# Optimization experiments

Measured on AMD Instinct MI355X. Metric: run time of the kernel, lower is better.

Reference implementation:

```python
import jax, jax.numpy as jnp
import numpy as np

N = 65536      # detector nodes (hits)
P = 128        # particles
DIM = 3
N_NEAREST = 5
EPS = 1e-8
BIG = 999.0


def setup_inputs() -> dict:
    key = jax.random.key(0)
    ks = jax.random.split(key, 9)
    x = jax.random.normal(ks[0], (N, DIM), jnp.float32)
    q = jax.random.uniform(ks[1], (N,), jnp.float32)
    is_cond_point = (jax.random.uniform(ks[2], (N,)) < 0.2).astype(jnp.float32)
    beta = jax.random.uniform(ks[3], (N,), jnp.float32)
    node_class = jax.random.randint(ks[4], (N,), 0, 6).astype(jnp.float32)
    max_x = jax.random.normal(ks[5], (P, DIM), jnp.float32)
    max_q = jax.random.uniform(ks[6], (P,), jnp.float32) + 0.5
    particle_class = jax.random.randint(ks[7], (P,), 0, 6).astype(jnp.float32)
    parent_target = jax.random.randint(ks[8], (N,), 0, P, dtype=jnp.int32)
    particle_idx = jnp.arange(P, dtype=jnp.int32)
    return dict(x=x, q=q, is_cond_point=is_cond_point, beta=beta,
                node_class=node_class, max_x=max_x, max_q=max_q,
                particle_class=particle_class, parent_target=parent_target,
                particle_idx=particle_idx)


def _rms_stats(dx, dxq, belongs, q_mailbox, cond_dist):
    # dx/dxq/belongs/cond_dist: [C, N] mailboxes (C receivers, each sees all N nodes)
    Np = belongs.sum(axis=1)                                   # [C]
    rms = jnp.sqrt(jnp.sum((dx * belongs) ** 2, axis=1) / Np)
    sum_q = jnp.sum(q_mailbox)  # NOTE: original sums the ENTIRE mailbox (quirk kept)
    rmsq = jnp.sqrt(jnp.sum(dxq ** 2, axis=1) / (Np * sum_q))
    cond = jnp.where(cond_dist < EPS, BIG, cond_dist)
    nn = -jax.lax.top_k(-cond, N_NEAREST)[0]  # 5 smallest, ascending == sort+slice
    return rms, rmsq, Np, nn


def reference(x, q, is_cond_point, beta, node_class, max_x, max_q, particle_class,
              parent_target, particle_idx):
    # --- update_all node_to_particle (message_dist -> compute_rms) ---
    dx = jnp.linalg.norm(x[None, :, :] - max_x[:, None, :], axis=-1)          # [P,N]
    belongs = (parent_target[None, :] == particle_idx[:, None]).astype(dx.dtype)
    dxq = dx * q[None, :] * max_q[:, None]
    cond = dx * is_cond_point[None, :]
    q_mb = jnp.broadcast_to(q[None, :], dx.shape)
    rms, rmsq, Np, nn = _rms_stats(dx, dxq, belongs, q_mb, cond)

    # --- update_all nodes->global (dst lacks 'max x'/'max q'/'particle idx') ---
    dxg = jnp.linalg.norm(x, axis=-1)[None, :]                                # [1,N]
    dxqg = dxg * q[None, :]
    belongs_g = jnp.ones_like(dxg)
    cond_g = dxg * is_cond_point[None, :]
    rms_g, rmsq_g, Ng, nn_g = _rms_stats(dxg, dxqg, belongs_g, q[None, :], cond_g)

    # --- update_all particles->global: Davies-Bouldin over [P,P] pairs ---
    DS = rms[:, None] + rms[None, :]                                          # Si+Sj
    M2 = jnp.sum((max_x[:, None, :] - max_x[None, :, :]) ** 2, axis=-1)       # ||xi-xj||^2
    R = jnp.where(M2 > 0, DS / jnp.where(M2 > 0, M2, 1.0), 0.0)               # nan/inf->0
    db = jnp.mean(jnp.max(R, axis=1))                                         # (1/P) sum_i max_j

    # --- update_all particle_to_node: node inherits its parent particle's N ---
    N_node = jnp.einsum('pn,p->n', belongs, Np)                               # [N]

    # --- apply_edges particle_to_node: ||max_x_p - x_n|| and membership ---
    dist_edge = dx            # [P,N], identical math to edges' 'dist x'
    belongs_edge = belongs    # [P,N]; beta/class edge feats are pure broadcasts

    return (rms, rmsq, Np, nn, rms_g, rmsq_g, Ng, nn_g, db,
            N_node, dist_edge, belongs_edge)
```

## Files before the change

### kernel.cpp

```cpp
#include <hip/hip_runtime.h>

#define NN 65536
#define PP 128
#define EPSV 1e-8f
#define BIGV 999.0f
#define MAGIC 0x7FEDC123

typedef float f32x4 __attribute__((ext_vector_type(4)));
typedef int   i32x4 __attribute__((ext_vector_type(4)));

#define O_RMS   0
#define O_RMSQ  128
#define O_NP    256
#define O_NN    384
#define O_RMSG  1024
#define O_RMSQG 1025
#define O_NG    1026
#define O_NNG   1027
#define O_DB    1032
#define O_NNODE 1033
#define O_DIST  66569
#define O_BEL   (66569 + 8388608)

#define W_BS   0
#define W_PP   512
#define W_CNT  41472
#define W_FLG  41536
#define W_CL4  41600

__device__ inline float wred(float v) {
#pragma unroll
  for (int o = 32; o > 0; o >>= 1) v += __shfl_down(v, o, 64);
  return v;
}

__device__ inline void t5ins(float t[5], float v) {
  if (v < t[4]) {
    t[4] = v;
#pragma unroll
    for (int k = 4; k > 0; --k)
      if (t[k] < t[k - 1]) { float tm = t[k]; t[k] = t[k - 1]; t[k - 1] = tm; }
  }
}

__device__ inline void merge5(const float* a, const float* b, float* o) {
  int i = 0, j = 0;
#pragma unroll
  for (int k = 0; k < 5; ++k) {
    float av = a[i], bv = b[j];
    if (av <= bv) { o[k] = av; ++i; } else { o[k] = bv; ++j; }
  }
}

__device__ inline void spin_flags(const int* flg, int tid) {
  if (tid < 64) {
    while (__hip_atomic_load(flg + tid, __ATOMIC_ACQUIRE,
                             __HIP_MEMORY_SCOPE_AGENT) != MAGIC)
      __builtin_amdgcn_s_sleep(2);
  }
  __syncthreads();
}

__global__ __launch_bounds__(256, 5) void gA(const float* __restrict__ x,
                                             const float* __restrict__ q,
                                             const float* __restrict__ ic,
                                             const int* __restrict__ par,
                                             const float* __restrict__ mx,
                                             const float* __restrict__ mq,
                                             float* __restrict__ ws,
                                             float* __restrict__ out) {
  __shared__ __align__(16) float sbuf[4132];
  int tid = threadIdx.x, bx = blockIdx.x;
  int* flg = (int*)ws + W_FLG;
  if (bx < 64) {
    float* ps = sbuf;
    float* wsum = sbuf + 640;
    int* swc = (int*)(sbuf + 672);
    int b = bx;
    for (int i = tid; i < 640; i += 256) ps[i] = 0.f;
    __syncthreads();
    float A = 0.f, B0 = 0.f, B1 = 0.f, B2 = 0.f, Cq = 0.f, Sq = 0.f, Sxx = 0.f;
    float4* cl4 = (float4*)(ws + W_CL4);
    int base = b * 1024;
    int wv = tid >> 6, lane = tid & 63;
    int running = 0;
    int pas[4];
#pragma unroll
    for (int it = 0; it < 4; ++it) {
      int n = base + it * 256 + tid;
      float x0 = x[3 * n], x1 = x[3 * n + 1], x2 = x[3 * n + 2];
      float qn = q[n], icn = ic[n];
      int pa = par[n];
      pas[it] = pa;
      float xx = fmaf(x0, x0, fmaf(x1, x1, x2 * x2));
      float q2 = qn * qn;
      A = fmaf(q2, xx, A); B0 = fmaf(q2, x0, B0);
      B1 = fmaf(q2, x1, B1); B2 = fmaf(q2, x2, B2);
      Cq += q2; Sq += qn; Sxx += xx;
      atomicAdd(&ps[pa], x0);
      atomicAdd(&ps[128 + pa], x1);
      atomicAdd(&ps[256 + pa], x2);
      atomicAdd(&ps[384 + pa], xx);
      atomicAdd(&ps[512 + pa], 1.0f);
      bool has = (icn != 0.0f);
      unsigned long long m = __ballot(has);
      if (lane == 0) swc[wv] = __popcll(m);
      __syncthreads();
      int c0 = swc[0], c1 = swc[1], c2 = swc[2], c3 = swc[3];
      int wbase = running + ((wv > 0) ? c0 : 0) + ((wv > 1) ? c1 : 0) + ((wv > 2) ? c2 : 0);
      if (has) {
        int pre = __popcll(m & ((1ull << lane) - 1ull));
        cl4[base + wbase + pre] = make_float4(x0, x1, x2, icn);
      }
      running += c0 + c1 + c2 + c3;
      __syncthreads();
    }
    A = wred(A); B0 = wred(B0); B1 = wred(B1); B2 = wred(B2);
    Cq = wred(Cq); Sq = wred(Sq); Sxx = wred(Sxx);
    if (lane == 0) {
      wsum[wv * 8 + 0] = A; wsum[wv * 8 + 1] = B0; wsum[wv * 8 + 2] = B1;
      wsum[wv * 8 + 3] = B2; wsum[wv * 8 + 4] = Cq; wsum[wv * 8 + 5] = Sq;
      wsum[wv * 8 + 6] = Sxx;
    }
    __syncthreads();
    if (tid < 7)
      ws[W_BS + b * 8 + tid] =
          wsum[tid] + wsum[8 + tid] + wsum[16 + tid] + wsum[24 + tid];
    if (tid == 0) ((int*)ws)[W_CNT + b] = running;
    for (int i = tid; i < 640; i += 256) ws[W_PP + b * 640 + i] = ps[i];
    __threadfence();
    __syncthreads();
    if (tid == 0)
      __hip_atomic_store(flg + b, MAGIC, __ATOMIC_RELEASE, __HIP_MEMORY_SCOPE_AGENT);
    spin_flags(flg, tid);
    float* snp = sbuf;
    if (tid < 128) {
      float s = 0.f;
      for (int b2 = 0; b2 < 64; ++b2) s += ws[W_PP + b2 * 640 + 512 + tid];
      snp[tid] = s;
    }
    __syncthreads();
#pragma unroll
    for (int it = 0; it < 4; ++it) {
      int n = base + it * 256 + tid;
      __builtin_nontemporal_store(snp[pas[it]], out + O_NNODE + n);
    }
  } else if (bx < 1088) {
    float* sx = sbuf;
    int* spar = (int*)(sbuf + 3080);
    float* smx = sbuf + 4108;
    int e = bx - 64;
    int ey = e >> 6, ex = e & 63;
    int p0 = ey * 8;
    if (tid < 24) smx[tid] = mx[p0 * 3 + tid];
    for (int i = tid; i < 770; i += 256) {
      int g4 = 768 * ex + 2 + i;
      if (g4 < 49152) *(f32x4*)(sx + 4 * i) = ((const f32x4*)x)[g4];
    }
    for (int i = tid; i < 257; i += 256) {
      int g4 = 256 * ex + i;
      if (g4 < 16384) *(i32x4*)(spar + 4 * i) = ((const i32x4*)par)[g4];
    }
    __syncthreads();
    int v = ex * 256 + tid;
    if (v < 16383) {
      int n0 = 3 + 4 * v;
      int lx = 1 + 12 * tid;
      float xv[12];
#pragma unroll
      for (int j = 0; j < 12; ++j) xv[j] = sx[lx + j];
      int lp = 3 + 4 * tid;
      int pa0 = spar[lp], pa1 = spar[lp + 1], pa2 = spar[lp + 2], pa3 = spar[lp + 3];
#pragma unroll
      for (int pi = 0; pi < 8; ++pi) {
        int p = p0 + pi;
        float m0 = smx[3 * pi], m1 = smx[3 * pi + 1], m2 = smx[3 * pi + 2];
        f32x4 d, bl;
        float d0, d1, d2;
        d0 = xv[0] - m0; d1 = xv[1] - m1; d2 = xv[2] - m2;
        d.x = sqrtf(fmaf(d0, d0, fmaf(d1, d1, d2 * d2)));
        d0 = xv[3] - m0; d1 = xv[4] - m1; d2 = xv[5] - m2;
        d.y = sqrtf(fmaf(d0, d0, fmaf(d1, d1, d2 * d2)));
        d0 = xv[6] - m0; d1 = xv[7] - m1; d2 = xv[8] - m2;
        d.z = sqrtf(fmaf(d0, d0, fmaf(d1, d1, d2 * d2)));
        d0 = xv[9] - m0; d1 = xv[10] - m1; d2 = xv[11] - m2;
        d.w = sqrtf(fmaf(d0, d0, fmaf(d1, d1, d2 * d2)));
        bl.x = (pa0 == p) ? 1.f : 0.f; bl.y = (pa1 == p) ? 1.f : 0.f;
        bl.z = (pa2 == p) ? 1.f : 0.f; bl.w = (pa3 == p) ? 1.f : 0.f;
        size_t ro = (size_t)p * NN + n0;
        __builtin_nontemporal_store(d,  (f32x4*)(out + O_DIST + ro));
        __builtin_nontemporal_store(bl, (f32x4*)(out + O_BEL + ro));
      }
    } else if (v == 16383) {
      float xs[4][3];
      int pa_r[4];
      int ns[4] = {0, 1, 2, 65535};
#pragma unroll
      for (int k = 0; k < 3; ++k) {
        xs[k][0] = x[3 * k]; xs[k][1] = x[3 * k + 1]; xs[k][2] = x[3 * k + 2];
        pa_r[k] = par[k];
      }
      xs[3][0] = sx[3061]; xs[3][1] = sx[3062]; xs[3][2] = sx[3063];
      pa_r[3] = spar[1023];
#pragma unroll
      for (int k = 0; k < 4; ++k) {
#pragma unroll
        for (int pi = 0; pi < 8; ++pi) {
          int p = p0 + pi;
          float m0 = smx[3 * pi], m1 = smx[3 * pi + 1], m2 = smx[3 * pi + 2];
          float d0 = xs[k][0] - m0, d1 = xs[k][1] - m1, d2 = xs[k][2] - m2;
          float dd = sqrtf(fmaf(d0, d0, fmaf(d1, d1, d2 * d2)));
          size_t ro = (size_t)p * NN + ns[k];
          __builtin_nontemporal_store(dd, out + O_DIST + ro);
          __builtin_nontemporal_store((pa_r[k] == p) ? 1.f : 0.f, out + O_BEL + ro);
        }
      }
    }
  } else {
    int r = bx - 1088;
    spin_flags(flg, tid);
    if (r < 129) {
      int* cnts = (int*)sbuf;
      float* sl = sbuf + 64;
      float m0 = 0.f, m1 = 0.f, m2 = 0.f;
      if (r < 128) { m0 = mx[3 * r]; m1 = mx[3 * r + 1]; m2 = mx[3 * r + 2]; }
      if (tid < 64) cnts[tid] = ((const int*)ws)[W_CNT + tid];
      __syncthreads();
      const float4* cl4 = (const float4*)(ws + W_CL4);
      float t[5] = {BIGV, BIGV, BIGV, BIGV, BIGV};
      for (int seg = 0; seg < 64; ++seg) {
        int c = cnts[seg];
        for (int i = tid; i < c; i += 256) {
          float4 e = cl4[seg * 1024 + i];
          float d0 = e.x - m0, d1 = e.y - m1, d2 = e.z - m2;
          float dd = sqrtf(fmaf(d0, d0, fmaf(d1, d1, d2 * d2)));
          float vv = dd * e.w;
          vv = (vv < EPSV) ? BIGV : vv;
          t5ins(t, vv);
        }
      }
#pragma unroll
      for (int k = 0; k < 5; ++k) sl[tid * 5 + k] = t[k];
      __syncthreads();
      for (int s = 128; s >= 1; s >>= 1) {
        if (tid < s) {
          float a[5], b[5], o[5];
#pragma unroll
          for (int k = 0; k < 5; ++k) { a[k] = sl[tid * 5 + k]; b[k] = sl[(tid + s) * 5 + k]; }
          merge5(a, b, o);
#pragma unroll
          for (int k = 0; k < 5; ++k) sl[tid * 5 + k] = o[k];
        }
        __syncthreads();
      }
      if (tid == 0) {
        float* dst = (r < 128) ? (out + O_NN + 5 * r) : (out + O_NNG);
#pragma unroll
        for (int k = 0; k < 5; ++k) dst[k] = sl[k];
      }
    } else {
      float* gs = sbuf;
      float* srms = sbuf + 8;
      float* smx2 = sbuf + 136;
      float* wsum2 = sbuf + 520;
      if (tid < 64) {
        float a0 = ws[W_BS + tid * 8 + 0], a1 = ws[W_BS + tid * 8 + 1];
        float a2 = ws[W_BS + tid * 8 + 2], a3 = ws[W_BS + tid * 8 + 3];
        float a4 = ws[W_BS + tid * 8 + 4], a5 = ws[W_BS + tid * 8 + 5];
        float a6 = ws[W_BS + tid * 8 + 6];
        a0 = wred(a0); a1 = wred(a1); a2 = wred(a2); a3 = wred(a3);
        a4 = wred(a4); a5 = wred(a5); a6 = wred(a6);
        if (tid == 0) {
          gs[0] = a0; gs[1] = a1; gs[2] = a2; gs[3] = a3;
          gs[4] = a4; gs[5] = a5; gs[6] = a6;
        }
      }
      __syncthreads();
      int p = tid;
      float rms = 0.f, m0 = 0.f, m1 = 0.f, m2 = 0.f;
      if (p < 128) {
        float A = gs[0], B0 = gs[1], B1 = gs[2], B2 = gs[3];
        float Cq = gs[4], Sq = gs[5];
        float sx0 = 0.f, sx1 = 0.f, sx2 = 0.f, sxx = 0.f, cnt = 0.f;
        for (int b = 0; b < 64; ++b) {
          const float* pp = ws + W_PP + b * 640;
          sx0 += pp[p]; sx1 += pp[128 + p]; sx2 += pp[256 + p];
          sxx += pp[384 + p]; cnt += pp[512 + p];
        }
        m0 = mx[3 * p]; m1 = mx[3 * p + 1]; m2 = mx[3 * p + 2];
        float mqv = mq[p];
        float mm = fmaf(m0, m0, fmaf(m1, m1, m2 * m2));
        float s1 = fmaxf(sxx - 2.f * (m0 * sx0 + m1 * sx1 + m2 * sx2) + mm * cnt, 0.f);
        rms = sqrtf(s1 / cnt);
        float s2 = fmaxf(A - 2.f * (m0 * B0 + m1 * B1 + m2 * B2) + mm * Cq, 0.f);
        float rmsq = sqrtf(mqv * mqv * s2 / (cnt * ((float)PP * Sq)));
        out[O_RMS + p] = rms; out[O_RMSQ + p] = rmsq; out[O_NP + p] = cnt;
        if (p == 0) {
          out[O_RMSG]  = sqrtf(gs[6] / (float)NN);
          out[O_RMSQG] = sqrtf(gs[0] / ((float)NN * Sq));
          out[O_NG]    = (float)NN;
        }
        srms[p] = rms;
        smx2[3 * p] = m0; smx2[3 * p + 1] = m1; smx2[3 * p + 2] = m2;
      }
      __syncthreads();
      if (p < 128) {
        float mr = 0.f;
        for (int j = 0; j < PP; ++j) {
          float d0 = m0 - smx2[3 * j], d1 = m1 - smx2[3 * j + 1], d2 = m2 - smx2[3 * j + 2];
          float M2 = fmaf(d0, d0, fmaf(d1, d1, d2 * d2));
          float rr = (M2 > 0.f) ? (rms + srms[j]) / M2 : 0.f;
          mr = fmaxf(mr, rr);
        }
        float sred = wred(mr);
        if ((p & 63) == 0) wsum2[p >> 6] = sred;
      }
      __syncthreads();
      if (tid == 0) out[O_DB] = (wsum2[0] + wsum2[1]) * (1.0f / 128.0f);
    }
  }
}

extern "C" void kernel_launch(void* const* d_in, const int* in_sizes, int n_in,
                              void* d_out, int out_size, void* d_ws, size_t ws_size,
                              hipStream_t stream) {
  const float* x  = (const float*)d_in[0];
  const float* q  = (const float*)d_in[1];
  const float* ic = (const float*)d_in[2];
  const float* mx = (const float*)d_in[5];
  const float* mq = (const float*)d_in[6];
  const int*   par = (const int*)d_in[8];
  float* out = (float*)d_out;
  float* ws = (float*)d_ws;

  hipLaunchKernelGGL(gA, dim3(1218), dim3(256), 0, stream,
                     x, q, ic, par, mx, mq, ws, out);
}
```

Measured before the change: 68.19 us.

## Drop LDS staging in dist tiles and use atomic compaction for cond points

The distance/belongs tiles now read x and parent indices directly from global memory instead of staging them through shared memory, which shrinks the LDS footprint from about 16.5KB to about 5KB and removes the forced occupancy hint. The cond-point compaction switches from a ballot-prefix scheme with two barriers per iteration to a shared atomic counter, and the compaction workspace offset moves. The intent is to raise occupancy and remove barriers. In exchange, the global x loads are strided and less coalesced, and the order of compacted cond points becomes nondeterministic within a block, which a 5-smallest search should tolerate.

Result: faster. 62.08 us (-9.0%).

```diff
diff --git a/kernel.cpp b/kernel.cpp
--- a/kernel.cpp
+++ b/kernel.cpp
@@ -7,7 +7,6 @@
 #define MAGIC 0x7FEDC123
 
 typedef float f32x4 __attribute__((ext_vector_type(4)));
-typedef int   i32x4 __attribute__((ext_vector_type(4)));
 
 #define O_RMS   0
 #define O_RMSQ  128
@@ -26,7 +25,7 @@
 #define W_PP   512
 #define W_CNT  41472
 #define W_FLG  41536
-#define W_CL4  41600
+#define W_CL4  303680
 
 __device__ inline float wred(float v) {
 #pragma unroll
@@ -61,29 +60,28 @@
   __syncthreads();
 }
 
-__global__ __launch_bounds__(256, 5) void gA(const float* __restrict__ x,
-                                             const float* __restrict__ q,
-                                             const float* __restrict__ ic,
-                                             const int* __restrict__ par,
-                                             const float* __restrict__ mx,
-                                             const float* __restrict__ mq,
-                                             float* __restrict__ ws,
-                                             float* __restrict__ out) {
-  __shared__ __align__(16) float sbuf[4132];
+__global__ __launch_bounds__(256) void gA(const float* __restrict__ x,
+                                          const float* __restrict__ q,
+                                          const float* __restrict__ ic,
+                                          const int* __restrict__ par,
+                                          const float* __restrict__ mx,
+                                          const float* __restrict__ mq,
+                                          float* __restrict__ ws,
+                                          float* __restrict__ out) {
+  __shared__ __align__(16) float sbuf[1344];
   int tid = threadIdx.x, bx = blockIdx.x;
   int* flg = (int*)ws + W_FLG;
   if (bx < 64) {
     float* ps = sbuf;
     float* wsum = sbuf + 640;
-    int* swc = (int*)(sbuf + 672);
+    int* lcnt = (int*)(sbuf + 672);
     int b = bx;
     for (int i = tid; i < 640; i += 256) ps[i] = 0.f;
+    if (tid == 0) *lcnt = 0;
     __syncthreads();
     float A = 0.f, B0 = 0.f, B1 = 0.f, B2 = 0.f, Cq = 0.f, Sq = 0.f, Sxx = 0.f;
     float4* cl4 = (float4*)(ws + W_CL4);
     int base = b * 1024;
-    int wv = tid >> 6, lane = tid & 63;
-    int running = 0;
     int pas[4];
 #pragma unroll
     for (int it = 0; it < 4; ++it) {
@@ -102,31 +100,24 @@
       atomicAdd(&ps[256 + pa], x2);
       atomicAdd(&ps[384 + pa], xx);
       atomicAdd(&ps[512 + pa], 1.0f);
-      bool has = (icn != 0.0f);
-      unsigned long long m = __ballot(has);
-      if (lane == 0) swc[wv] = __popcll(m);
-      __syncthreads();
-      int c0 = swc[0], c1 = swc[1], c2 = swc[2], c3 = swc[3];
-      int wbase = running + ((wv > 0) ? c0 : 0) + ((wv > 1) ? c1 : 0) + ((wv > 2) ? c2 : 0);
-      if (has) {
-        int pre = __popcll(m & ((1ull << lane) - 1ull));
-        cl4[base + wbase + pre] = make_float4(x0, x1, x2, icn);
-      }
-      running += c0 + c1 + c2 + c3;
-      __syncthreads();
+      if (icn != 0.0f) {
+        int loc = atomicAdd(lcnt, 1);
+        cl4[base + loc] = make_float4(x0, x1, x2, icn);
+      }
     }
     A = wred(A); B0 = wred(B0); B1 = wred(B1); B2 = wred(B2);
     Cq = wred(Cq); Sq = wred(Sq); Sxx = wred(Sxx);
+    int w = tid >> 6, lane = tid & 63;
     if (lane == 0) {
-      wsum[wv * 8 + 0] = A; wsum[wv * 8 + 1] = B0; wsum[wv * 8 + 2] = B1;
-      wsum[wv * 8 + 3] = B2; wsum[wv * 8 + 4] = Cq; wsum[wv * 8 + 5] = Sq;
-      wsum[wv * 8 + 6] = Sxx;
+      wsum[w * 8 + 0] = A; wsum[w * 8 + 1] = B0; wsum[w * 8 + 2] = B1;
+      wsum[w * 8 + 3] = B2; wsum[w * 8 + 4] = Cq; wsum[w * 8 + 5] = Sq;
+      wsum[w * 8 + 6] = Sxx;
     }
     __syncthreads();
     if (tid < 7)
       ws[W_BS + b * 8 + tid] =
           wsum[tid] + wsum[8 + tid] + wsum[16 + tid] + wsum[24 + tid];
-    if (tid == 0) ((int*)ws)[W_CNT + b] = running;
+    if (tid == 0) ((int*)ws)[W_CNT + b] = *lcnt;
     for (int i = tid; i < 640; i += 256) ws[W_PP + b * 640 + i] = ps[i];
     __threadfence();
     __syncthreads();
@@ -146,31 +137,19 @@
       __builtin_nontemporal_store(snp[pas[it]], out + O_NNODE + n);
     }
   } else if (bx < 1088) {
-    float* sx = sbuf;
-    int* spar = (int*)(sbuf + 3080);
-    float* smx = sbuf + 4108;
+    float* smx = sbuf;
     int e = bx - 64;
     int ey = e >> 6, ex = e & 63;
     int p0 = ey * 8;
     if (tid < 24) smx[tid] = mx[p0 * 3 + tid];
-    for (int i = tid; i < 770; i += 256) {
-      int g4 = 768 * ex + 2 + i;
-      if (g4 < 49152) *(f32x4*)(sx + 4 * i) = ((const f32x4*)x)[g4];
-    }
-    for (int i = tid; i < 257; i += 256) {
-      int g4 = 256 * ex + i;
-      if (g4 < 16384) *(i32x4*)(spar + 4 * i) = ((const i32x4*)par)[g4];
-    }
     __syncthreads();
     int v = ex * 256 + tid;
     if (v < 16383) {
       int n0 = 3 + 4 * v;
-      int lx = 1 + 12 * tid;
       float xv[12];
 #pragma unroll
-      for (int j = 0; j < 12; ++j) xv[j] = sx[lx + j];
-      int lp = 3 + 4 * tid;
-      int pa0 = spar[lp], pa1 = spar[lp + 1], pa2 = spar[lp + 2], pa3 = spar[lp + 3];
+      for (int j = 0; j < 12; ++j) xv[j] = x[3 * n0 + j];
+      int pa0 = par[n0], pa1 = par[n0 + 1], pa2 = par[n0 + 2], pa3 = par[n0 + 3];
 #pragma unroll
       for (int pi = 0; pi < 8; ++pi) {
         int p = p0 + pi;
@@ -192,27 +171,21 @@
         __builtin_nontemporal_store(bl, (f32x4*)(out + O_BEL + ro));
       }
     } else if (v == 16383) {
-      float xs[4][3];
-      int pa_r[4];
       int ns[4] = {0, 1, 2, 65535};
 #pragma unroll
-      for (int k = 0; k < 3; ++k) {
-        xs[k][0] = x[3 * k]; xs[k][1] = x[3 * k + 1]; xs[k][2] = x[3 * k + 2];
-        pa_r[k] = par[k];
-      }
-      xs[3][0] = sx[3061]; xs[3][1] = sx[3062]; xs[3][2] = sx[3063];
-      pa_r[3] = spar[1023];
-#pragma unroll
       for (int k = 0; k < 4; ++k) {
+        int n = ns[k];
+        float x0 = x[3 * n], x1 = x[3 * n + 1], x2 = x[3 * n + 2];
+        int pa = par[n];
 #pragma unroll
         for (int pi = 0; pi < 8; ++pi) {
           int p = p0 + pi;
           float m0 = smx[3 * pi], m1 = smx[3 * pi + 1], m2 = smx[3 * pi + 2];
-          float d0 = xs[k][0] - m0, d1 = xs[k][1] - m1, d2 = xs[k][2] - m2;
+          float d0 = x0 - m0, d1 = x1 - m1, d2 = x2 - m2;
           float dd = sqrtf(fmaf(d0, d0, fmaf(d1, d1, d2 * d2)));
-          size_t ro = (size_t)p * NN + ns[k];
+          size_t ro = (size_t)p * NN + n;
           __builtin_nontemporal_store(dd, out + O_DIST + ro);
-          __builtin_nontemporal_store((pa_r[k] == p) ? 1.f : 0.f, out + O_BEL + ro);
+          __builtin_nontemporal_store((pa == p) ? 1.f : 0.f, out + O_BEL + ro);
         }
       }
     }
```
